# Optimization experiments

Hardware: AMD Instinct MI355X
Metric: run time of the kernel (lower is better)

Reference implementation:

```python
import jax, jax.numpy as jnp
import numpy as np

NUM_CLASSES = 80
STRIDES = (8, 16, 32)
FEAT_HW = ((80, 80), (40, 40), (20, 20))
B = 32
MAX_GT = 60


def setup_inputs() -> dict:
    key = jax.random.key(0)
    ks = jax.random.split(key, 6)
    feats = {}
    for i, (s, (h, w)) in enumerate(zip(STRIDES, FEAT_HW)):
        feats[f"feat{s}"] = jax.random.normal(ks[i], (B, 5 + NUM_CLASSES, h, w), jnp.float32)
    u = jax.random.uniform(ks[3], (B, MAX_GT, 4), jnp.float32)
    # cx,cy in [0,640), w,h in [8,128): realistic pixel-space gt boxes for a 640x640 image
    gt_boxes = jnp.concatenate([u[..., :2] * 640.0, u[..., 2:] * 120.0 + 8.0], -1)
    gt_classes = jax.random.randint(ks[4], (B, MAX_GT), 0, NUM_CLASSES)
    num_gts = jax.random.randint(ks[5], (B,), 1, MAX_GT + 1)
    return dict(feat8=feats["feat8"], feat16=feats["feat16"], feat32=feats["feat32"],
                gt_boxes=gt_boxes, gt_classes=gt_classes, num_gts=num_gts)


def _decode(feat, stride):
    # torch get_output_and_grid: xy=(raw+grid)*stride, wh=exp(raw)*stride
    b, c, h, w = feat.shape
    yv, xv = jnp.meshgrid(jnp.arange(h), jnp.arange(w), indexing="ij")
    gx = xv.reshape(-1).astype(feat.dtype)  # [H*W]
    gy = yv.reshape(-1).astype(feat.dtype)
    out = feat.reshape(b, c, h * w).transpose(0, 2, 1)  # [B,A,C]
    xy = (out[..., :2] + jnp.stack([gx, gy], -1)[None]) * stride
    wh = jnp.exp(out[..., 2:4]) * stride
    return jnp.concatenate([xy, wh, out[..., 4:]], -1), gx, gy


def _pair_iou(a, b):
    # a: [G,4] xywh, b: [A,4] xywh -> [G,A] IoU (bboxes_iou, xyxy=False)
    tl = jnp.maximum(a[:, None, :2] - a[:, None, 2:] * 0.5, b[None, :, :2] - b[None, :, 2:] * 0.5)
    br = jnp.minimum(a[:, None, :2] + a[:, None, 2:] * 0.5, b[None, :, :2] + b[None, :, 2:] * 0.5)
    en = jnp.all(tl < br, -1)
    inter = jnp.where(en, jnp.prod(br - tl, -1), 0.0)
    area_a = jnp.prod(a[:, 2:], -1)
    area_b = jnp.prod(b[:, 2:], -1)
    return inter / (area_a[:, None] + area_b[None, :] - inter + 1e-16)


def _bce_logits(x, t):
    return jnp.maximum(x, 0.0) - x * t + jnp.log1p(jnp.exp(-jnp.abs(x)))


def _iou_loss(pred, tgt):
    # IOUloss(loss_type='iou'): 1 - iou^2, per box
    tl = jnp.maximum(pred[..., :2] - pred[..., 2:] * 0.5, tgt[..., :2] - tgt[..., 2:] * 0.5)
    br = jnp.minimum(pred[..., :2] + pred[..., 2:] * 0.5, tgt[..., :2] + tgt[..., 2:] * 0.5)
    en = jnp.all(tl < br, -1)
    inter = jnp.where(en, jnp.prod(br - tl, -1), 0.0)
    union = jnp.prod(pred[..., 2:], -1) + jnp.prod(tgt[..., 2:], -1) - inter
    iou = inter / (union + 1e-16)
    return 1.0 - iou ** 2


def _assign(boxes, cls_lo, obj_lo, gtb, gtc, vmask, cx, cy, st):
    # SimOTA per image. boxes [A,4], cls_lo [A,C], obj_lo [A], gtb [G,4], gtc [G] int,
    # vmask [G] bool (gt padding), cx/cy/st [A] anchor centers & strides.
    G, A = gtb.shape[0], boxes.shape[0]
    iou = _pair_iou(gtb, boxes)  # [G,A]
    gx, gy = gtb[:, :1], gtb[:, 1:2]
    gw, gh = gtb[:, 2:3], gtb[:, 3:4]
    in_box = ((cx[None] > gx - 0.5 * gw) & (cx[None] < gx + 0.5 * gw) &
              (cy[None] > gy - 0.5 * gh) & (cy[None] < gy + 0.5 * gh))
    R = 2.5  # center sampling radius (in strides)
    in_ctr = ((cx[None] > gx - R * st[None]) & (cx[None] < gx + R * st[None]) &
              (cy[None] > gy - R * st[None]) & (cy[None] < gy + R * st[None]))
    fg = ((in_box | in_ctr) & vmask[:, None]).any(0)  # [A] candidate anchors
    in_both = (in_box & in_ctr).astype(boxes.dtype)
    # pairwise cls cost: BCE(sqrt(sig(cls)*sig(obj)), onehot(gt_cls)).sum(-1),
    # decomposed to avoid the [G,A,C] tensor: sum_c bce0 + (bce1-bce0)[gt_cls]
    p = jnp.clip(jnp.sqrt(jax.nn.sigmoid(cls_lo) * jax.nn.sigmoid(obj_lo)[:, None]), 1e-7, 1.0 - 1e-7)
    bce1 = -jnp.log(p)          # [A,C]
    bce0 = -jnp.log(1.0 - p)    # [A,C]
    cls_cost = bce0.sum(-1)[None, :] + (bce1 - bce0)[:, gtc].T  # [G,A]
    cost = (cls_cost + 3.0 * (-jnp.log(iou + 1e-8))
            + 100000.0 * (1.0 - in_both)
            + 1e9 * (~fg)[None, :].astype(boxes.dtype)
            + 1e9 * (~vmask)[:, None].astype(boxes.dtype))
    K = 10  # n_candidate_k
    topk_ious, _ = jax.lax.top_k(iou * fg[None, :], K)
    dyn_k = jnp.maximum(topk_ious.sum(-1).astype(jnp.int32), 1)  # clamp(int(sum), min=1)
    _, pos = jax.lax.top_k(-cost, K)  # [G,K] lowest-cost anchors per gt
    sel = (jnp.arange(K)[None, :] < dyn_k[:, None]).astype(boxes.dtype)
    matching = jnp.zeros((G, A), boxes.dtype).at[jnp.arange(G)[:, None], pos].set(sel)
    matching = matching * vmask[:, None].astype(boxes.dtype)
    # resolve anchors claimed by >1 gt: keep min-cost gt
    conflict = matching.sum(0) > 1
    best_gt = jnp.argmin(cost, axis=0)  # [A]
    matching = jnp.where(conflict[None, :], jax.nn.one_hot(best_gt, G, dtype=matching.dtype).T, matching)
    fg_final = matching.sum(0) > 0  # [A]
    matched = jnp.argmax(matching, axis=0)  # [A]
    pred_iou = (matching * iou).sum(0)  # [A]
    cls_t = jax.nn.one_hot(gtc[matched], NUM_CLASSES, dtype=boxes.dtype) * pred_iou[:, None]
    reg_t = gtb[matched]
    return fg_final, cls_t, reg_t


def _forward(feat8, feat16, feat32, gt_boxes, gt_classes, num_gts):
    outs, cxs, cys, sts = [], [], [], []
    for f, s in zip((feat8, feat16, feat32), STRIDES):
        o, gx, gy = _decode(f, float(s))
        outs.append(o)
        cxs.append((gx + 0.5) * s)
        cys.append((gy + 0.5) * s)
        sts.append(jnp.full_like(gx, s))
    preds = jnp.concatenate(outs, 1)  # [B,A,5+C]
    cx = jnp.concatenate(cxs)
    cy = jnp.concatenate(cys)
    st = jnp.concatenate(sts)
    boxes = preds[..., :4]
    obj_lo = preds[..., 4]
    cls_lo = preds[..., 5:]
    vmask = jnp.arange(MAX_GT)[None, :] < num_gts[:, None]
    fg, cls_t, reg_t = jax.vmap(_assign, in_axes=(0, 0, 0, 0, 0, 0, None, None, None))(
        boxes, cls_lo, obj_lo, gt_boxes, gt_classes, vmask, cx, cy, st)
    # SimOTA assignment is no_grad in YOLOX: targets are constants wrt preds
    fg = jax.lax.stop_gradient(fg)
    cls_t = jax.lax.stop_gradient(cls_t)
    reg_t = jax.lax.stop_gradient(reg_t)
    fg_f = fg.astype(boxes.dtype)
    num_fg = jnp.maximum(fg_f.sum(), 1.0)
    loss_iou = (_iou_loss(boxes, reg_t) * fg_f).sum()
    loss_obj = _bce_logits(obj_lo, fg_f * 0.9).sum()  # obj_targets * 0.9 smoothing
    loss_cls = (_bce_logits(cls_lo, cls_t) * fg_f[..., None]).sum()
    REG_WEIGHT = 5.0
    return (REG_WEIGHT * loss_iou + loss_obj + loss_cls) / num_fg


def reference(feat8, feat16, feat32, gt_boxes, gt_classes, num_gts):
    return _forward(feat8, feat16, feat32, gt_boxes, gt_classes, num_gts)
```

## Files before the change

### kernel.cpp

```cpp
#include <hip/hip_runtime.h>

constexpr int kB = 32;
constexpr int kA = 8400;
constexpr int kG = 60;
constexpr int kC = 80;
constexpr int kK = 10;
constexpr int kNBx = (kA + 255)/256;
constexpr int kNB = kNBx * kB;

__device__ __forceinline__ float fexp(float x){ return __expf(x); }
__device__ __forceinline__ float flog(float x){ return __logf(x); }
__device__ __forceinline__ float frcp(float x){ return __builtin_amdgcn_rcpf(x); }
__device__ __forceinline__ float frsq(float x){ return __builtin_amdgcn_rsqf(x); }
__device__ __forceinline__ float fsqrt(float x){ return __builtin_amdgcn_sqrtf(x); }
__device__ __forceinline__ float fdiv(float a, float b){ return a * __builtin_amdgcn_rcpf(b); }
__device__ __forceinline__ float sigm(float x){ return frcp(1.0f + fexp(-x)); }
__device__ __forceinline__ float bce(float x, float t){
  return fmaxf(x, 0.0f) - x*t + flog(1.0f + fexp(-fabsf(x)));
}

__device__ __forceinline__ unsigned ordbits(float v){
  unsigned u = __float_as_uint(v);
  return (u & 0x80000000u) ? ~u : (u | 0x80000000u);
}
__device__ __forceinline__ float unpackf(unsigned k){
  return __uint_as_float((k & 0x80000000u) ? (k & 0x7fffffffu) : ~k);
}

struct AInfo { int x, y; float st; };
__device__ __forceinline__ AInfo ainfo(int a){
  AInfo r;
  if (a < 6400)      { r.x = a % 80;           r.y = a / 80;           r.st = 8.0f;  }
  else if (a < 8000) { int l = a-6400; r.x = l % 40; r.y = l / 40;     r.st = 16.0f; }
  else               { int l = a-8000; r.x = l % 20; r.y = l / 20;     r.st = 32.0f; }
  return r;
}

__device__ __forceinline__ float featv(const float* __restrict__ f8,
                                       const float* __restrict__ f16,
                                       const float* __restrict__ f32x,
                                       int b, int ch, int a){
  if (a < 6400) return f8 [(b*85 + ch)*6400 + a];
  if (a < 8000) return f16[(b*85 + ch)*1600 + (a - 6400)];
  return             f32x[(b*85 + ch)*400  + (a - 8000)];
}

__device__ __forceinline__ float pair_iou(float4 g, float4 p){
  float tlx = fmaxf(g.x - g.z*0.5f, p.x - p.z*0.5f);
  float tly = fmaxf(g.y - g.w*0.5f, p.y - p.w*0.5f);
  float brx = fminf(g.x + g.z*0.5f, p.x + p.z*0.5f);
  float bry = fminf(g.y + g.w*0.5f, p.y + p.w*0.5f);
  float inter = (tlx < brx && tly < bry) ? (brx-tlx)*(bry-tly) : 0.0f;
  return fdiv(inter, g.z*g.w + p.z*p.w - inter + 1e-16f);
}

__device__ __forceinline__ float cost_core(float iou, float cl, float obs, float b0sum,
                                           int a, float4 gt, int fg_a){
  AInfo ai = ainfo(a);
  float cx = ((float)ai.x + 0.5f)*ai.st;
  float cy = ((float)ai.y + 0.5f)*ai.st;
  bool in_box = (cx > gt.x - 0.5f*gt.z) && (cx < gt.x + 0.5f*gt.z)
             && (cy > gt.y - 0.5f*gt.w) && (cy < gt.y + 0.5f*gt.w);
  bool in_ctr = (cx > gt.x - 2.5f*ai.st) && (cx < gt.x + 2.5f*ai.st)
             && (cy > gt.y - 2.5f*ai.st) && (cy < gt.y + 2.5f*ai.st);
  float p = fsqrt(sigm(cl) * obs);
  p = fminf(fmaxf(p, 1e-7f), 1.0f - 1e-7f);
  float diff = -flog(p) + flog(1.0f - p);
  float c = b0sum + diff;
  c += 3.0f * (-flog(iou + 1e-8f));
  c += (in_box && in_ctr) ? 0.0f : 100000.0f;
  c += fg_a ? 0.0f : 1000000000.0f;
  return c;
}

__global__ __launch_bounds__(256) void k_decode(
    const float* __restrict__ f8, const float* __restrict__ f16, const float* __restrict__ f32x,
    const float* __restrict__ gtb, const int* __restrict__ ngts,
    float* __restrict__ boxes, float* __restrict__ objl, float* __restrict__ b0s,
    float* __restrict__ bceS, float* __restrict__ obsA,
    int* __restrict__ fg, int* __restrict__ cnt, int* __restrict__ mtch){
  int b = blockIdx.y;
  int tid = threadIdx.x;
  int a = blockIdx.x*256 + tid;
  __shared__ float4 sg[kG];
  if (tid < kG) sg[tid] = ((const float4*)gtb)[b*kG + tid];
  __syncthreads();
  if (a >= kA) return;
  int ng = ngts[b];
  const float* base; int hw, off; float st_; int gx, gy;
  if (a < 6400)      { base=f8;   hw=6400; off=a;        st_=8.0f;  gx=off%80; gy=off/80; }
  else if (a < 8000) { base=f16;  hw=1600; off=a-6400;   st_=16.0f; gx=off%40; gy=off/40; }
  else               { base=f32x; hw=400;  off=a-8000;   st_=32.0f; gx=off%20; gy=off/20; }
  const float* p0 = base + ((size_t)b*85)*hw + off;
  float t0 = p0[0];
  float t1 = p0[(size_t)hw];
  float t2 = p0[(size_t)2*hw];
  float t3 = p0[(size_t)3*hw];
  float ob = p0[(size_t)4*hw];
  float4 bx;
  bx.x = (t0 + (float)gx) * st_;
  bx.y = (t1 + (float)gy) * st_;
  bx.z = fexp(t2) * st_;
  bx.w = fexp(t3) * st_;
  int idx = b*kA + a;
  ((float4*)boxes)[idx] = bx;
  objl[idx] = ob;
  float obs = sigm(ob);
  obsA[idx] = obs;
  float so = fsqrt(obs);
  float s = 0.0f;
  float sumCl = 0.0f;
  float slogv = 0.0f;
  const float* pc = p0 + (size_t)5*hw;
  #pragma unroll 2
  for (int grp = 0; grp < kC/8; ++grp){
    float prodS = 1.0f, prodV = 1.0f;
    #pragma unroll
    for (int j = 0; j < 8; ++j){
      float cl = pc[(size_t)(grp*8 + j)*hw];
      float u = fexp(-cl);
      float v = 1.0f + u;
      float p = so * frsq(v);
      p = fminf(fmaxf(p, 1e-7f), 1.0f - 1e-7f);
      prodS *= (1.0f - p);
      prodV *= v;
      sumCl += cl;
    }
    s -= flog(prodS);
    slogv += flog(prodV);
  }
  b0s[idx] = s;
  bceS[idx] = sumCl + slogv;
  float cx = ((float)gx + 0.5f)*st_;
  float cy = ((float)gy + 0.5f)*st_;
  int f = 0;
  for (int g = 0; g < ng; ++g){
    float4 gt = sg[g];
    bool in_box = (cx > gt.x - 0.5f*gt.z) && (cx < gt.x + 0.5f*gt.z)
               && (cy > gt.y - 0.5f*gt.w) && (cy < gt.y + 0.5f*gt.w);
    bool in_ctr = (cx > gt.x - 2.5f*st_) && (cx < gt.x + 2.5f*st_)
               && (cy > gt.y - 2.5f*st_) && (cy < gt.y + 2.5f*st_);
    if (in_box || in_ctr){ f = 1; break; }
  }
  fg[idx] = f;
  cnt[idx] = 0;
  mtch[idx] = 0x7fffffff;
}

__global__ __launch_bounds__(1024) void k_compact(
    const int* __restrict__ fg, unsigned short* __restrict__ alist, int* __restrict__ mcnt){
  int b = blockIdx.x;
  int tid = threadIdx.x;
  const int CH = 9;
  int start = tid*CH;
  int myf[CH]; int cl = 0;
  #pragma unroll
  for (int j = 0; j < CH; ++j){
    int a = start + j;
    int f = (a < kA) ? fg[b*kA + a] : 0;
    myf[j] = f; cl += f;
  }
  __shared__ int s1[1024], s2[1024];
  int* cur = s1; int* nxt = s2;
  cur[tid] = cl; __syncthreads();
  for (int off = 1; off < 1024; off <<= 1){
    int v = cur[tid];
    if (tid >= off) v += cur[tid - off];
    nxt[tid] = v; __syncthreads();
    int* t = cur; cur = nxt; nxt = t;
  }
  int o = cur[tid] - cl;
  unsigned short* out = alist + (size_t)b*kA;
  #pragma unroll
  for (int j = 0; j < CH; ++j){
    int a = start + j;
    if (a < kA && myf[j]) out[o++] = (unsigned short)a;
  }
  if (tid == 1023) mcnt[b] = cur[tid];
}

__global__ __launch_bounds__(256) void k_assign(
    const float* __restrict__ f8, const float* __restrict__ f16, const float* __restrict__ f32x,
    const float* __restrict__ gtb, const int* __restrict__ gtc, const int* __restrict__ ngts,
    const float* __restrict__ boxes, const float* __restrict__ obsA, const float* __restrict__ b0s,
    const int* __restrict__ fg, const unsigned short* __restrict__ alist, const int* __restrict__ mcnt,
    int* __restrict__ cnt, int* __restrict__ mtch){
  int b = blockIdx.x / kG;
  int g = blockIdx.x % kG;
  if (g >= ngts[b]) return;
  int tid = threadIdx.x;
  int lane = tid & 63, wid = tid >> 6;
  float4 gt = ((const float4*)gtb)[b*kG + g];
  int cls = gtc[b*kG + g];
  const float4* bx4 = (const float4*)boxes;
  const float* c8  = f8   + ((size_t)b*85 + 5 + cls)*6400;
  const float* c16 = f16  + ((size_t)b*85 + 5 + cls)*1600;
  const float* c32 = f32x + ((size_t)b*85 + 5 + cls)*400;
  int m = mcnt[b];
  bool full = (m < kK);
  int len = full ? kA : m;
  const unsigned short* al = alist + (size_t)b*kA;
  __shared__ unsigned long long wk[4];

  unsigned long long k1[kK], k2[kK];
  #pragma unroll
  for (int i = 0; i < kK; ++i){ k1[i] = 0ull; k2[i] = 0ull; }

  for (int i = tid; i < len; i += 256){
    int a = full ? i : (int)al[i];
    int idx = b*kA + a;
    float4 bx = bx4[idx];
    float iou = pair_iou(gt, bx);
    int fga = full ? fg[idx] : 1;
    float v = fga ? iou : 0.0f;
    unsigned long long key1 = ((unsigned long long)ordbits(v) << 32) | (unsigned)(~a);
    if (key1 > k1[kK-1]){
      k1[kK-1] = key1;
      #pragma unroll
      for (int i2 = kK-1; i2 > 0; --i2)
        if (k1[i2] > k1[i2-1]){ unsigned long long t = k1[i2]; k1[i2] = k1[i2-1]; k1[i2-1] = t; }
    }
    float cl = (a < 6400) ? c8[a] : (a < 8000) ? c16[a-6400] : c32[a-8000];
    float c = cost_core(iou, cl, obsA[idx], b0s[idx], a, gt, fga);
    unsigned long long key2 = ~(((unsigned long long)ordbits(c) << 32) | (unsigned)a);
    if (key2 > k2[kK-1]){
      k2[kK-1] = key2;
      #pragma unroll
      for (int i2 = kK-1; i2 > 0; --i2)
        if (k2[i2] > k2[i2-1]){ unsigned long long t = k2[i2]; k2[i2] = k2[i2-1]; k2[i2-1] = t; }
    }
  }

  float ksum = 0.0f;
  for (int k = 0; k < kK; ++k){
    unsigned long long best = k1[0];
    #pragma unroll
    for (int off = 32; off; off >>= 1){
      unsigned long long o = __shfl_xor(best, off, 64);
      if (o > best) best = o;
    }
    if (lane == 0) wk[wid] = best;
    __syncthreads();
    unsigned long long w0 = wk[0];
    if (wk[1] > w0) w0 = wk[1];
    if (wk[2] > w0) w0 = wk[2];
    if (wk[3] > w0) w0 = wk[3];
    if (k1[0] == w0){
      #pragma unroll
      for (int i = 0; i < kK-1; ++i) k1[i] = k1[i+1];
      k1[kK-1] = 0ull;
    }
    ksum += unpackf((unsigned)(w0 >> 32));
    __syncthreads();
  }
  int dynk = max((int)ksum, 1);

  int my_a = -1;
  for (int k = 0; k < kK; ++k){
    unsigned long long best = k2[0];
    #pragma unroll
    for (int off = 32; off; off >>= 1){
      unsigned long long o = __shfl_xor(best, off, 64);
      if (o > best) best = o;
    }
    if (lane == 0) wk[wid] = best;
    __syncthreads();
    unsigned long long w0 = wk[0];
    if (wk[1] > w0) w0 = wk[1];
    if (wk[2] > w0) w0 = wk[2];
    if (wk[3] > w0) w0 = wk[3];
    if (k2[0] == w0){
      #pragma unroll
      for (int i = 0; i < kK-1; ++i) k2[i] = k2[i+1];
      k2[kK-1] = 0ull;
    }
    if (tid == k) my_a = (int)((unsigned)(~w0) & 0xffffffffu);
    __syncthreads();
  }
  if (tid < kK && tid < dynk){
    atomicAdd(&cnt[b*kA + my_a], 1);
    atomicMin(&mtch[b*kA + my_a], g);
  }
}

__global__ __launch_bounds__(256) void k_loss(
    const float* __restrict__ f8, const float* __restrict__ f16, const float* __restrict__ f32x,
    const float* __restrict__ gtb, const int* __restrict__ gtc, const int* __restrict__ ngts,
    const float* __restrict__ boxes, const float* __restrict__ objl, const float* __restrict__ b0s,
    const float* __restrict__ bceS, const float* __restrict__ obsA,
    const int* __restrict__ fg, const int* __restrict__ cnt, const int* __restrict__ mtch,
    float4* __restrict__ pacc){
  int b = blockIdx.y;
  int a = blockIdx.x*256 + threadIdx.x;
  int tid = threadIdx.x;
  __shared__ float4 sg[kG];
  __shared__ int scls[kG];
  if (tid < kG){ sg[tid] = ((const float4*)gtb)[b*kG + tid]; scls[tid] = gtc[b*kG + tid]; }
  __syncthreads();
  float li = 0.0f, lo = 0.0f, lc = 0.0f, nf = 0.0f;
  bool valid = (a < kA);
  int idx = valid ? (b*kA + a) : (b*kA);
  int c = valid ? cnt[idx] : 0;
  float ob = valid ? objl[idx] : 0.0f;
  float4 bx = valid ? ((const float4*)boxes)[idx] : make_float4(0,0,1,1);

  float fgf = 0.0f; int mg = 0;
  if (valid && c == 1){ mg = mtch[idx]; fgf = 1.0f; }
  bool need = valid && (c > 1);
  if (__any(need)){
    if (need){
      int ng = ngts[b];
      float b0 = b0s[idx];
      float obs = obsA[idx];
      int fga = fg[idx];
      float bestc = 3.0e38f; int bg = 0;
      for (int g = 0; g < ng; ++g){
        float iou = pair_iou(sg[g], bx);
        float cl = featv(f8,f16,f32x,b,5+scls[g],a);
        float cst = cost_core(iou, cl, obs, b0, a, sg[g], fga);
        if (cst < bestc){ bestc = cst; bg = g; }
      }
      mg = bg; fgf = 1.0f;
    }
  }
  if (valid){
    lo = bce(ob, fgf*0.9f);
    if (fgf > 0.0f){
      nf = 1.0f;
      float4 r = sg[mg];
      float piou = pair_iou(r, bx);
      float tlx = fmaxf(bx.x - bx.z*0.5f, r.x - r.z*0.5f);
      float tly = fmaxf(bx.y - bx.w*0.5f, r.y - r.w*0.5f);
      float brx = fminf(bx.x + bx.z*0.5f, r.x + r.z*0.5f);
      float bry = fminf(bx.y + bx.w*0.5f, r.y + r.w*0.5f);
      float inter = (tlx < brx && tly < bry) ? (brx-tlx)*(bry-tly) : 0.0f;
      float un = bx.z*bx.w + r.z*r.w - inter;
      float iou = fdiv(inter, un + 1e-16f);
      li = 1.0f - iou*iou;
      int tc = scls[mg];
      float cl_tc = featv(f8,f16,f32x,b,5+tc,a);
      lc = bceS[idx] - piou * cl_tc;
    }
  }
  for (int off = 32; off > 0; off >>= 1){
    li += __shfl_down(li, off, 64);
    lo += __shfl_down(lo, off, 64);
    lc += __shfl_down(lc, off, 64);
    nf += __shfl_down(nf, off, 64);
  }
  __shared__ float4 wred[4];
  int wid = tid >> 6;
  if ((tid & 63) == 0) wred[wid] = make_float4(li, lo, lc, nf);
  __syncthreads();
  if (tid == 0){
    float4 t = wred[0];
    for (int w = 1; w < 4; ++w){
      float4 o = wred[w];
      t.x += o.x; t.y += o.y; t.z += o.z; t.w += o.w;
    }
    pacc[blockIdx.y * gridDim.x + blockIdx.x] = t;
  }
}

__global__ __launch_bounds__(256) void k_final(
    const float4* __restrict__ pacc, float* __restrict__ out){
  int tid = threadIdx.x;
  float li = 0.0f, lo = 0.0f, lc = 0.0f, nf = 0.0f;
  for (int i = tid; i < kNB; i += 256){
    float4 p = pacc[i];
    li += p.x; lo += p.y; lc += p.z; nf += p.w;
  }
  for (int off = 32; off > 0; off >>= 1){
    li += __shfl_down(li, off, 64);
    lo += __shfl_down(lo, off, 64);
    lc += __shfl_down(lc, off, 64);
    nf += __shfl_down(nf, off, 64);
  }
  __shared__ float4 wred[4];
  int wid = tid >> 6;
  if ((tid & 63) == 0) wred[wid] = make_float4(li, lo, lc, nf);
  __syncthreads();
  if (tid == 0){
    float4 t = wred[0];
    for (int w = 1; w < 4; ++w){
      float4 o = wred[w];
      t.x += o.x; t.y += o.y; t.z += o.z; t.w += o.w;
    }
    out[0] = (5.0f*t.x + t.y + t.z) * frcp(fmaxf(t.w, 1.0f));
  }
}

extern "C" void kernel_launch(void* const* d_in, const int* in_sizes, int n_in,
                              void* d_out, int out_size, void* d_ws, size_t ws_size,
                              hipStream_t stream) {
  (void)in_sizes; (void)n_in; (void)out_size; (void)ws_size;
  const float* f8   = (const float*)d_in[0];
  const float* f16  = (const float*)d_in[1];
  const float* f32x = (const float*)d_in[2];
  const float* gtb  = (const float*)d_in[3];
  const int*   gtc  = (const int*)d_in[4];
  const int*   ngts = (const int*)d_in[5];
  float* out = (float*)d_out;

  const size_t BA = (size_t)kB*kA;
  float* ws    = (float*)d_ws;
  float* boxes = ws;
  float* objl  = boxes + BA*4;
  float* b0s   = objl  + BA;
  float* bceS  = b0s   + BA;
  float* obsA  = bceS  + BA;
  int*   fg    = (int*)(obsA + BA);
  int*   cnt   = fg  + BA;
  int*   mtch  = cnt + BA;
  unsigned short* alist = (unsigned short*)(mtch + BA);
  int*   mcnt  = (int*)(alist + BA);
  float4* pacc = (float4*)(mcnt + kB);

  dim3 gBA(kNBx, kB);
  k_decode<<<gBA, dim3(256), 0, stream>>>(f8,f16,f32x,gtb,ngts,boxes,objl,b0s,bceS,obsA,fg,cnt,mtch);
  k_compact<<<dim3(kB), dim3(1024), 0, stream>>>(fg, alist, mcnt);
  k_assign<<<dim3(kB*kG), dim3(256), 0, stream>>>(f8,f16,f32x,gtb,gtc,ngts,boxes,obsA,b0s,fg,alist,mcnt,cnt,mtch);
  k_loss<<<gBA, dim3(256), 0, stream>>>(f8,f16,f32x,gtb,gtc,ngts,boxes,objl,b0s,bceS,obsA,fg,cnt,mtch,pacc);
  k_final<<<dim3(1), dim3(256), 0, stream>>>(pacc, out);
}
```

Before: 216.3 us.

## Restructure SimOTA top-k merge and skip cost eval for anchors outside box-and-center

In the per-GT assignment kernel, the cost top-k on the compacted candidate list now only evaluates anchors that fall inside both the GT box and its center region. It falls back to a full second pass over the candidates when fewer than k such anchors exist. The cross-wave top-k merge is also changed: each wave extracts its own top 10 with shuffles only, writes them to shared memory, and a single wave merges the 40 candidates. This replaces 20 rounds of block-wide __syncthreads. The goal is to cut the cost computation and global loads for anchors that cannot win, and to remove barrier overhead, at the price of a possible second pass and more shared memory.

Measured after the change: 223.2 us. 3.2% more time.

```diff
diff --git a/kernel.cpp b/kernel.cpp
--- a/kernel.cpp
+++ b/kernel.cpp
@@ -71,6 +71,15 @@
   c += (in_box && in_ctr) ? 0.0f : 100000.0f;
   c += fg_a ? 0.0f : 1000000000.0f;
   return c;
+}
+
+__device__ __forceinline__ void insert10(unsigned long long* arr, unsigned long long key){
+  if (key > arr[kK-1]){
+    arr[kK-1] = key;
+    #pragma unroll
+    for (int i = kK-1; i > 0; --i)
+      if (arr[i] > arr[i-1]){ unsigned long long t = arr[i]; arr[i] = arr[i-1]; arr[i-1] = t; }
+  }
 }
 
 __global__ __launch_bounds__(256) void k_decode(
@@ -197,41 +206,69 @@
   const float* c16 = f16  + ((size_t)b*85 + 5 + cls)*1600;
   const float* c32 = f32x + ((size_t)b*85 + 5 + cls)*400;
   int m = mcnt[b];
-  bool full = (m < kK);
-  int len = full ? kA : m;
+  bool full0 = (m < kK);
+  int len = full0 ? kA : m;
   const unsigned short* al = alist + (size_t)b*kA;
-  __shared__ unsigned long long wk[4];
+
+  __shared__ unsigned long long stop1[4][kK], stop2[4][kK];
+  __shared__ int swb[4];
 
   unsigned long long k1[kK], k2[kK];
   #pragma unroll
   for (int i = 0; i < kK; ++i){ k1[i] = 0ull; k2[i] = 0ull; }
+  int nboth = 0;
 
   for (int i = tid; i < len; i += 256){
-    int a = full ? i : (int)al[i];
+    int a = full0 ? i : (int)al[i];
     int idx = b*kA + a;
     float4 bx = bx4[idx];
     float iou = pair_iou(gt, bx);
-    int fga = full ? fg[idx] : 1;
-    float v = fga ? iou : 0.0f;
-    unsigned long long key1 = ((unsigned long long)ordbits(v) << 32) | (unsigned)(~a);
-    if (key1 > k1[kK-1]){
-      k1[kK-1] = key1;
-      #pragma unroll
-      for (int i2 = kK-1; i2 > 0; --i2)
-        if (k1[i2] > k1[i2-1]){ unsigned long long t = k1[i2]; k1[i2] = k1[i2-1]; k1[i2-1] = t; }
-    }
-    float cl = (a < 6400) ? c8[a] : (a < 8000) ? c16[a-6400] : c32[a-8000];
-    float c = cost_core(iou, cl, obsA[idx], b0s[idx], a, gt, fga);
-    unsigned long long key2 = ~(((unsigned long long)ordbits(c) << 32) | (unsigned)a);
-    if (key2 > k2[kK-1]){
-      k2[kK-1] = key2;
-      #pragma unroll
-      for (int i2 = kK-1; i2 > 0; --i2)
-        if (k2[i2] > k2[i2-1]){ unsigned long long t = k2[i2]; k2[i2] = k2[i2-1]; k2[i2-1] = t; }
-    }
-  }
-
-  float ksum = 0.0f;
+    if (full0){
+      int fga = fg[idx];
+      float v = fga ? iou : 0.0f;
+      insert10(k1, ((unsigned long long)ordbits(v) << 32) | (unsigned)(~a));
+      float cl = (a < 6400) ? c8[a] : (a < 8000) ? c16[a-6400] : c32[a-8000];
+      float c = cost_core(iou, cl, obsA[idx], b0s[idx], a, gt, fga);
+      insert10(k2, ~(((unsigned long long)ordbits(c) << 32) | (unsigned)a));
+    } else {
+      insert10(k1, ((unsigned long long)ordbits(iou) << 32) | (unsigned)(~a));
+      AInfo ai = ainfo(a);
+      float cx = ((float)ai.x + 0.5f)*ai.st;
+      float cy = ((float)ai.y + 0.5f)*ai.st;
+      bool in_box = (cx > gt.x - 0.5f*gt.z) && (cx < gt.x + 0.5f*gt.z)
+                 && (cy > gt.y - 0.5f*gt.w) && (cy < gt.y + 0.5f*gt.w);
+      bool in_ctr = (cx > gt.x - 2.5f*ai.st) && (cx < gt.x + 2.5f*ai.st)
+                 && (cy > gt.y - 2.5f*ai.st) && (cy < gt.y + 2.5f*ai.st);
+      if (in_box && in_ctr){
+        ++nboth;
+        float cl = (a < 6400) ? c8[a] : (a < 8000) ? c16[a-6400] : c32[a-8000];
+        float c = cost_core(iou, cl, obsA[idx], b0s[idx], a, gt, 1);
+        insert10(k2, ~(((unsigned long long)ordbits(c) << 32) | (unsigned)a));
+      }
+    }
+  }
+
+  int nb = nboth;
+  #pragma unroll
+  for (int off = 32; off; off >>= 1) nb += __shfl_down(nb, off, 64);
+  if (lane == 0) swb[wid] = nb;
+  __syncthreads();
+  int sboth = swb[0] + swb[1] + swb[2] + swb[3];
+
+  if (!full0 && sboth < kK){
+    #pragma unroll
+    for (int i = 0; i < kK; ++i) k2[i] = 0ull;
+    for (int i = tid; i < len; i += 256){
+      int a = (int)al[i];
+      int idx = b*kA + a;
+      float iou = pair_iou(gt, bx4[idx]);
+      float cl = (a < 6400) ? c8[a] : (a < 8000) ? c16[a-6400] : c32[a-8000];
+      float c = cost_core(iou, cl, obsA[idx], b0s[idx], a, gt, 1);
+      insert10(k2, ~(((unsigned long long)ordbits(c) << 32) | (unsigned)a));
+    }
+  }
+
+  #pragma unroll 1
   for (int k = 0; k < kK; ++k){
     unsigned long long best = k1[0];
     #pragma unroll
@@ -239,23 +276,14 @@
       unsigned long long o = __shfl_xor(best, off, 64);
       if (o > best) best = o;
     }
-    if (lane == 0) wk[wid] = best;
-    __syncthreads();
-    unsigned long long w0 = wk[0];
-    if (wk[1] > w0) w0 = wk[1];
-    if (wk[2] > w0) w0 = wk[2];
-    if (wk[3] > w0) w0 = wk[3];
-    if (k1[0] == w0){
+    if (k1[0] == best){
       #pragma unroll
       for (int i = 0; i < kK-1; ++i) k1[i] = k1[i+1];
       k1[kK-1] = 0ull;
     }
-    ksum += unpackf((unsigned)(w0 >> 32));
-    __syncthreads();
-  }
-  int dynk = max((int)ksum, 1);
-
-  int my_a = -1;
+    if (lane == 0) stop1[wid][k] = best;
+  }
+  #pragma unroll 1
   for (int k = 0; k < kK; ++k){
     unsigned long long best = k2[0];
     #pragma unroll
@@ -263,23 +291,47 @@
       unsigned long long o = __shfl_xor(best, off, 64);
       if (o > best) best = o;
     }
-    if (lane == 0) wk[wid] = best;
-    __syncthreads();
-    unsigned long long w0 = wk[0];
-    if (wk[1] > w0) w0 = wk[1];
-    if (wk[2] > w0) w0 = wk[2];
-    if (wk[3] > w0) w0 = wk[3];
-    if (k2[0] == w0){
+    if (k2[0] == best){
       #pragma unroll
       for (int i = 0; i < kK-1; ++i) k2[i] = k2[i+1];
       k2[kK-1] = 0ull;
     }
-    if (tid == k) my_a = (int)((unsigned)(~w0) & 0xffffffffu);
-    __syncthreads();
-  }
-  if (tid < kK && tid < dynk){
-    atomicAdd(&cnt[b*kA + my_a], 1);
-    atomicMin(&mtch[b*kA + my_a], g);
+    if (lane == 0) stop2[wid][k] = best;
+  }
+  __syncthreads();
+
+  if (wid == 0){
+    unsigned long long cand1 = (lane < 40) ? stop1[lane/kK][lane % kK] : 0ull;
+    unsigned long long cand2 = (lane < 40) ? stop2[lane/kK][lane % kK] : 0ull;
+    float ksum = 0.0f;
+    #pragma unroll 1
+    for (int k = 0; k < kK; ++k){
+      unsigned long long best = cand1;
+      #pragma unroll
+      for (int off = 32; off; off >>= 1){
+        unsigned long long o = __shfl_xor(best, off, 64);
+        if (o > best) best = o;
+      }
+      if (cand1 == best) cand1 = 0ull;
+      ksum += unpackf((unsigned)(best >> 32));
+    }
+    int dynk = max((int)ksum, 1);
+    int my_a = -1;
+    #pragma unroll 1
+    for (int k = 0; k < kK; ++k){
+      unsigned long long best = cand2;
+      #pragma unroll
+      for (int off = 32; off; off >>= 1){
+        unsigned long long o = __shfl_xor(best, off, 64);
+        if (o > best) best = o;
+      }
+      if (cand2 == best) cand2 = 0ull;
+      if (lane == k) my_a = (int)((unsigned)(~best) & 0xffffffffu);
+    }
+    if (lane < kK && lane < dynk){
+      atomicAdd(&cnt[b*kA + my_a], 1);
+      atomicMin(&mtch[b*kA + my_a], g);
+    }
   }
 }
 
```
